# Performance work log

Hardware: AMD Instinct MI355X
Metric: run time of the kernel (lower is better)

The kernel has to match this reference:

```python
import jax, jax.numpy as jnp
import numpy as np

N = 16384
D = 512
K = 1024          # fixed num_clusters (torch code uses randint(2, N//2))
NUM_ITERS = 10    # kmeans Lloyd iterations
NUM_CLUSTER_ITERS = 1
TEMPERATURE = 0.1
CONCENTRATION = 0.1
EPS = 1e-6


def setup_inputs() -> dict:
    key = jax.random.key(0)
    feats = jax.random.normal(key, (N, D), dtype=jnp.float32)
    return {"feats": feats}


def _assign(feats, centroids, x_sq):
    c_sq = jnp.sum(centroids * centroids, axis=-1)            # [K]
    d = x_sq[:, None] - 2.0 * (feats @ centroids.T) + c_sq[None, :]
    return jnp.argmin(d, axis=-1)                             # [N] int32


def _kmeans(feats, num_clusters, num_iters):
    x_sq = jnp.sum(feats * feats, axis=-1)                    # [N]
    init_centroids = feats[:num_clusters]                     # deterministic init

    def body(_, centroids):
        clusters = _assign(feats, centroids, x_sq)
        sums = jax.ops.segment_sum(feats, clusters, num_segments=num_clusters)
        counts = jax.ops.segment_sum(jnp.ones((feats.shape[0],), feats.dtype),
                                     clusters, num_segments=num_clusters)
        new_c = sums / jnp.maximum(counts, 1.0)[:, None]
        # keep old centroid for empty clusters
        return jnp.where(counts[:, None] > 0, new_c, centroids)

    centroids = jax.lax.fori_loop(0, num_iters, body, init_centroids)
    clusters = _assign(feats, centroids, x_sq)
    counts = jax.ops.segment_sum(jnp.ones((feats.shape[0],), feats.dtype),
                                 clusters, num_segments=num_clusters)
    return clusters, centroids, counts


def reference(feats):
    clusters, centroids, _ = _kmeans(feats, K, NUM_ITERS)
    # per-point squared residuals gathered by cluster id, scatter-added to [K, D]
    resid2 = (feats - centroids[clusters]) ** 2               # [N, D]
    dists = jax.ops.segment_sum(resid2, clusters, num_segments=K)  # [K, D]
    # entropy loss branch (concentration phi)
    p = jnp.exp(-dists / CONCENTRATION)
    Q = p / jnp.sum(p)
    entropy = jnp.mean(Q * jnp.log(Q + EPS)) / NUM_CLUSTER_ITERS
    # nll branch (temperature t)
    p2 = jnp.exp(-dists / TEMPERATURE)
    nll = -jnp.mean(jnp.log(p2 + EPS))
    return entropy + nll
```

## Files before the change

kernel.cpp:

```cpp
#include <hip/hip_runtime.h>
#include <math.h>

#define N 16384
#define D 512
#define K 1024
#define NUM_ITERS 10
#define TEMPERATURE 0.1f
#define CONCENTRATION 0.1f
#define EPS 1e-6f

typedef unsigned short ushort_t;
typedef unsigned int uint_t;
typedef unsigned long long u64;
typedef __attribute__((ext_vector_type(4))) float floatx4;
typedef __attribute__((ext_vector_type(8))) short shortx8;

#define BM 128
#define BN 128
#define BK 64

__device__ inline ushort_t f2h(float f) {
    _Float16 h = (_Float16)f;
    return *(ushort_t*)&h;
}

__device__ inline unsigned ford(float f) {
    unsigned b = __float_as_uint(f);
    return (b & 0x80000000u) ? ~b : (b | 0x80000000u);
}

__device__ inline void f4add(float4& a, const float4& b) {
    a.x += b.x; a.y += b.y; a.z += b.z; a.w += b.w;
}

__device__ inline void gld16(const void* g, void* l) {
    __builtin_amdgcn_global_load_lds(
        (const __attribute__((address_space(1))) void*)(uintptr_t)(g),
        (__attribute__((address_space(3))) void*)(uintptr_t)(l), 16, 0, 0);
}

__global__ void split_kernel(const float* __restrict__ x, ushort_t* __restrict__ hi,
                             u64* __restrict__ best2, int n4) {
    int i = blockIdx.x * 256 + threadIdx.x;
    if (i >= n4) return;
    float4 v = ((const float4*)x)[i];
    ushort4 hv = {f2h(v.x), f2h(v.y), f2h(v.z), f2h(v.w)};
    ((ushort4*)hi)[i] = hv;
    if (i < 2 * N) best2[i] = ~0ull;
}

__global__ void rowsq_kernel(const float* __restrict__ x, float* __restrict__ out, int rows) {
    int row = blockIdx.x * 4 + (threadIdx.x >> 6);
    int lane = threadIdx.x & 63;
    if (row >= rows) return;
    const float* r = x + (size_t)row * D;
    float s = 0.f;
    for (int i = lane; i < D; i += 64) { float v = r[i]; s += v * v; }
    for (int off = 32; off > 0; off >>= 1) s += __shfl_down(s, off, 64);
    if (lane == 0) out[row] = s;
}

__global__ __launch_bounds__(256) void assign_mfma(
    const ushort_t* __restrict__ Ah, const ushort_t* __restrict__ Bh,
    const float* __restrict__ csq, u64* __restrict__ best)
{
    __shared__ __align__(16) ushort_t sAh[BM * BK];
    __shared__ __align__(16) ushort_t sBh[BN * BK];

    const int tid = threadIdx.x;
    const int lane = tid & 63;
    const int wave = tid >> 6;
    const int wr = wave >> 1, wc = wave & 1;
    const int quad = lane >> 4, l16 = lane & 15;

    const int q = (int)blockIdx.x;
    const int xid = q & 7;
    const int s = q >> 3;
    const int brow = ((s >> 3) << 3) + xid;
    const int bcol = s & 7;
    const int row0 = brow * BM, col0 = bcol * BN;

    floatx4 acc[4][4];
#pragma unroll
    for (int a = 0; a < 4; ++a)
#pragma unroll
        for (int b = 0; b < 4; ++b) acc[a][b] = (floatx4){0.f, 0.f, 0.f, 0.f};

    const int r_s0 = tid >> 3;
    const int kb_s0 = tid & 7;

    for (int d0 = 0; d0 < D; d0 += BK) {
        __syncthreads();
#pragma unroll
        for (int i = 0; i < 4; ++i) {
            const int row = r_s0 + i * 32;
            const int kb = kb_s0 ^ (row & 7);
            const int dst = (i * 256 + tid) * 8;
            const size_t ga = (size_t)(row0 + row) * D + d0 + kb * 8;
            const size_t gb = (size_t)(col0 + row) * D + d0 + kb * 8;
            gld16(Ah + ga, sAh + dst);
            gld16(Bh + gb, sBh + dst);
        }
        __syncthreads();

#pragma unroll
        for (int c = 0; c < 2; ++c) {
            shortx8 fah[4], fbh[4];
#pragma unroll
            for (int t = 0; t < 4; ++t) {
                const int ar = wr * 64 + t * 16 + l16;
                const int bc = wc * 64 + t * 16 + l16;
                const int kbl = c * 4 + quad;
                const int qa = (kbl ^ (ar & 7)) * 8;
                const int qb = (kbl ^ (bc & 7)) * 8;
                fah[t] = *(const shortx8*)&sAh[ar * BK + qa];
                fbh[t] = *(const shortx8*)&sBh[bc * BK + qb];
            }
#pragma unroll
            for (int i = 0; i < 4; ++i)
#pragma unroll
                for (int j = 0; j < 4; ++j)
                    acc[i][j] = __builtin_amdgcn_mfma_f32_16x16x32_f16(fah[i], fbh[j], acc[i][j], 0, 0, 0);
        }
    }

    float csqv[4];
#pragma unroll
    for (int j = 0; j < 4; ++j) csqv[j] = csq[col0 + wc * 64 + j * 16 + l16];

    const int k0 = col0 + wc * 64 + l16;
#pragma unroll
    for (int i = 0; i < 4; ++i) {
#pragma unroll
        for (int r = 0; r < 4; ++r) {
            float bv = csqv[0] - 2.0f * acc[i][0][r];
            int bk = k0;
#pragma unroll
            for (int j = 1; j < 4; ++j) {
                float v = csqv[j] - 2.0f * acc[i][j][r];
                int kk = k0 + j * 16;
                if (v < bv || (v == bv && kk < bk)) { bv = v; bk = kk; }
            }
#pragma unroll
            for (int m = 1; m < 16; m <<= 1) {
                float ov = __shfl_xor(bv, m, 64);
                int ok = __shfl_xor(bk, m, 64);
                if (ov < bv || (ov == bv && ok < bk)) { bv = ov; bk = ok; }
            }
            if (l16 == 0) {
                int p = row0 + wr * 64 + i * 16 + quad * 4 + r;
                u64 pk = ((u64)ford(bv) << 32) | (unsigned)bk;
                atomicMin(&best[p], pk);
            }
        }
    }
}

#define CU_WAVES 8
#define CHUNKS (N / 128)
#define ROUNDS 4
#define WIN (CHUNKS / ROUNDS)
#define CPW (WIN / CU_WAVES)

__global__ __launch_bounds__(512) void cluster_update(
    const float* __restrict__ feats, const u64* __restrict__ best,
    u64* __restrict__ best_other,
    float* __restrict__ cent, ushort_t* __restrict__ Bh,
    float* __restrict__ csq)
{
    __shared__ int list[CU_WAVES][CPW * 128];
    __shared__ int lcnt[CU_WAVES];
    __shared__ float4 part[CU_WAVES][64][2];
    __shared__ int pcnt_s[CU_WAVES];

    const int tid = threadIdx.x;
    const int lane = tid & 63;
    const int wave = tid >> 6;
    const int k = (int)blockIdx.x;

    float4 a0 = {0.f, 0.f, 0.f, 0.f}, a1 = {0.f, 0.f, 0.f, 0.f};
    int cnttot = 0;

    for (int round = 0; round < ROUNDS; ++round) {
        int cw = 0;
#pragma unroll
        for (int cc = 0; cc < CPW; ++cc) {
            int chunk = round * WIN + wave * CPW + cc;
            ulonglong2 v = ((const ulonglong2*)best)[chunk * 64 + lane];
            int id0 = (int)(uint_t)v.x;
            int id1 = (int)(uint_t)v.y;
            int p0 = chunk * 128 + 2 * lane;
            u64 m0 = __ballot(id0 == k);
            u64 m1 = __ballot(id1 == k);
            int c0 = __popcll(m0);
            u64 lanem = (1ull << lane) - 1ull;
            if (id0 == k) list[wave][cw + __popcll(m0 & lanem)] = p0;
            if (id1 == k) list[wave][cw + c0 + __popcll(m1 & lanem)] = p0 + 1;
            cw += c0 + __popcll(m1);
        }
        if (lane == 0) lcnt[wave] = cw;
        cnttot += cw;
        __syncthreads();

        int off[CU_WAVES]; int T = 0;
#pragma unroll
        for (int j = 0; j < CU_WAVES; ++j) { off[j] = T; T += lcnt[j]; }

        for (int g0 = wave; g0 < T; g0 += CU_WAVES * 4) {
            int nb = 0; int pidx[4];
#pragma unroll
            for (int b = 0; b < 4; ++b) {
                int g = g0 + CU_WAVES * b;
                if (g < T) {
                    int j = 0;
#pragma unroll
                    for (int jj = 1; jj < CU_WAVES; ++jj) if (g >= off[jj]) j = jj;
                    pidx[nb++] = list[j][g - off[j]];
                }
            }
            float4 x[4][2];
#pragma unroll
            for (int b = 0; b < 4; ++b) if (b < nb) {
                const float4* r = (const float4*)(feats + (size_t)pidx[b] * D) + lane * 2;
                x[b][0] = r[0]; x[b][1] = r[1];
            }
#pragma unroll
            for (int b = 0; b < 4; ++b) if (b < nb) {
                f4add(a0, x[b][0]); f4add(a1, x[b][1]);
            }
        }
        __syncthreads();
    }

    part[wave][lane][0] = a0; part[wave][lane][1] = a1;
    if (lane == 0) pcnt_s[wave] = cnttot;
    __syncthreads();

    if (wave == 0) {
        float4 s0 = part[0][lane][0], s1 = part[0][lane][1];
        int c = pcnt_s[0];
#pragma unroll
        for (int w = 1; w < CU_WAVES; ++w) {
            f4add(s0, part[w][lane][0]); f4add(s1, part[w][lane][1]);
            c += pcnt_s[w];
        }

        float4* crow = (float4*)(cent + (size_t)k * D) + lane * 2;
        float4 c0, c1;
        if (c > 0) {
            float cf = (float)c;
            c0 = (float4){s0.x / cf, s0.y / cf, s0.z / cf, s0.w / cf};
            c1 = (float4){s1.x / cf, s1.y / cf, s1.z / cf, s1.w / cf};
        } else {
            c0 = crow[0]; c1 = crow[1];
        }
        crow[0] = c0; crow[1] = c1;

        ushort4 hv;
        hv.x = f2h(c0.x); hv.y = f2h(c0.y); hv.z = f2h(c0.z); hv.w = f2h(c0.w);
        ((ushort4*)(Bh + (size_t)k * D))[lane * 2] = hv;
        hv.x = f2h(c1.x); hv.y = f2h(c1.y); hv.z = f2h(c1.z); hv.w = f2h(c1.w);
        ((ushort4*)(Bh + (size_t)k * D))[lane * 2 + 1] = hv;

        float s = c0.x * c0.x + c0.y * c0.y + c0.z * c0.z + c0.w * c0.w
                + c1.x * c1.x + c1.y * c1.y + c1.z * c1.z + c1.w * c1.w;
        for (int o = 32; o > 0; o >>= 1) s += __shfl_xor(s, o, 64);
        if (lane == 0) csq[k] = s;
    }

    if (tid < 16) best_other[k * 16 + tid] = ~0ull;
}

__global__ __launch_bounds__(512) void dist_gather(
    const float* __restrict__ feats, const float* __restrict__ cent,
    const u64* __restrict__ best, float* __restrict__ dists)
{
    __shared__ int list[CU_WAVES][CPW * 128];
    __shared__ int lcnt[CU_WAVES];
    __shared__ float4 part[CU_WAVES][64][2];

    const int tid = threadIdx.x;
    const int lane = tid & 63;
    const int wave = tid >> 6;
    const int k = (int)blockIdx.x;

    const float4* crow = (const float4*)(cent + (size_t)k * D) + lane * 2;
    const float4 c0 = crow[0], c1 = crow[1];

    float4 a0 = {0.f, 0.f, 0.f, 0.f}, a1 = {0.f, 0.f, 0.f, 0.f};

    for (int round = 0; round < ROUNDS; ++round) {
        int cw = 0;
#pragma unroll
        for (int cc = 0; cc < CPW; ++cc) {
            int chunk = round * WIN + wave * CPW + cc;
            ulonglong2 v = ((const ulonglong2*)best)[chunk * 64 + lane];
            int id0 = (int)(uint_t)v.x;
            int id1 = (int)(uint_t)v.y;
            int p0 = chunk * 128 + 2 * lane;
            u64 m0 = __ballot(id0 == k);
            u64 m1 = __ballot(id1 == k);
            int cc0 = __popcll(m0);
            u64 lanem = (1ull << lane) - 1ull;
            if (id0 == k) list[wave][cw + __popcll(m0 & lanem)] = p0;
            if (id1 == k) list[wave][cw + cc0 + __popcll(m1 & lanem)] = p0 + 1;
            cw += cc0 + __popcll(m1);
        }
        if (lane == 0) lcnt[wave] = cw;
        __syncthreads();

        int off[CU_WAVES]; int T = 0;
#pragma unroll
        for (int j = 0; j < CU_WAVES; ++j) { off[j] = T; T += lcnt[j]; }

        for (int g0 = wave; g0 < T; g0 += CU_WAVES * 4) {
            int nb = 0; int pidx[4];
#pragma unroll
            for (int b = 0; b < 4; ++b) {
                int g = g0 + CU_WAVES * b;
                if (g < T) {
                    int j = 0;
#pragma unroll
                    for (int jj = 1; jj < CU_WAVES; ++jj) if (g >= off[jj]) j = jj;
                    pidx[nb++] = list[j][g - off[j]];
                }
            }
            float4 x[4][2];
#pragma unroll
            for (int b = 0; b < 4; ++b) if (b < nb) {
                const float4* r = (const float4*)(feats + (size_t)pidx[b] * D) + lane * 2;
                x[b][0] = r[0]; x[b][1] = r[1];
            }
#pragma unroll
            for (int b = 0; b < 4; ++b) if (b < nb) {
                float r;
                r = x[b][0].x - c0.x; a0.x += r * r;  r = x[b][0].y - c0.y; a0.y += r * r;
                r = x[b][0].z - c0.z; a0.z += r * r;  r = x[b][0].w - c0.w; a0.w += r * r;
                r = x[b][1].x - c1.x; a1.x += r * r;  r = x[b][1].y - c1.y; a1.y += r * r;
                r = x[b][1].z - c1.z; a1.z += r * r;  r = x[b][1].w - c1.w; a1.w += r * r;
            }
        }
        __syncthreads();
    }

    part[wave][lane][0] = a0; part[wave][lane][1] = a1;
    __syncthreads();
    if (wave == 0) {
        float4 s0 = part[0][lane][0], s1 = part[0][lane][1];
#pragma unroll
        for (int w = 1; w < CU_WAVES; ++w) { f4add(s0, part[w][lane][0]); f4add(s1, part[w][lane][1]); }
        float4* drow = (float4*)(dists + (size_t)k * D) + lane * 2;
        drow[0] = s0; drow[1] = s1;
    }
}

__global__ void sump_kernel(const float* __restrict__ dists, double* __restrict__ S) {
    int tid = threadIdx.x;
    float v = 0.f;
    for (int idx = blockIdx.x * 256 + tid; idx < K * D; idx += 256 * 256)
        v += expf(-(dists[idx] / CONCENTRATION));
    __shared__ float red[4];
    for (int off = 32; off > 0; off >>= 1) v += __shfl_down(v, off, 64);
    if ((tid & 63) == 0) red[tid >> 6] = v;
    __syncthreads();
    if (tid == 0) atomicAdd(S, (double)(red[0] + red[1] + red[2] + red[3]));
}

__global__ void loss_kernel(const float* __restrict__ dists, const double* __restrict__ Sd,
                            double* __restrict__ acc2) {
    int tid = threadIdx.x;
    float S = (float)Sd[0];
    float e = 0.f, nl = 0.f;
    for (int idx = blockIdx.x * 256 + tid; idx < K * D; idx += 256 * 256) {
        float dv = dists[idx];
        float p = expf(-(dv / CONCENTRATION));
        float qq = p / S;
        e += qq * logf(qq + EPS);
        float p2 = expf(-(dv / TEMPERATURE));
        nl += logf(p2 + EPS);
    }
    __shared__ float rede[4];
    __shared__ float redn[4];
    for (int off = 32; off > 0; off >>= 1) { e += __shfl_down(e, off, 64); nl += __shfl_down(nl, off, 64); }
    if ((tid & 63) == 0) { rede[tid >> 6] = e; redn[tid >> 6] = nl; }
    __syncthreads();
    if (tid == 0) {
        atomicAdd(&acc2[0], (double)(rede[0] + rede[1] + rede[2] + rede[3]));
        atomicAdd(&acc2[1], (double)(redn[0] + redn[1] + redn[2] + redn[3]));
    }
}

__global__ void finalize_kernel(const double* __restrict__ acc2, float* __restrict__ out) {
    double kd = (double)(K * D);
    double entropy = acc2[0] / kd;
    double nll = -(acc2[1] / kd);
    out[0] = (float)(entropy + nll);
}

extern "C" void kernel_launch(void* const* d_in, const int* in_sizes, int n_in,
                              void* d_out, int out_size, void* d_ws, size_t ws_size,
                              hipStream_t stream) {
    const float* feats = (const float*)d_in[0];
    float* out = (float*)d_out;

    ushort_t* Ah = (ushort_t*)d_ws;
    ushort_t* Bh = Ah + (size_t)N * D;
    float* centroids = (float*)(Bh + (size_t)K * D);
    float* dists     = centroids + (size_t)K * D;
    float* csq       = dists + (size_t)K * D;
    u64*   best0     = (u64*)(csq + K);
    u64*   best1     = best0 + N;
    double* scal     = (double*)(best1 + N);

    split_kernel<<<(N * D / 4) / 256, 256, 0, stream>>>(feats, Ah, best0, N * D / 4);
    hipMemcpyAsync(centroids, feats, (size_t)K * D * sizeof(float),
                   hipMemcpyDeviceToDevice, stream);
    rowsq_kernel<<<K / 4, 256, 0, stream>>>(feats, csq, K);

    for (int it = 0; it < NUM_ITERS; ++it) {
        u64* cur = (it & 1) ? best1 : best0;
        u64* oth = (it & 1) ? best0 : best1;
        const ushort_t* bh = (it == 0) ? Ah : Bh;
        assign_mfma<<<(N / BM) * (K / BN), 256, 0, stream>>>(Ah, bh, csq, cur);
        cluster_update<<<K, 512, 0, stream>>>(feats, cur, oth, centroids, Bh, csq);
    }
    u64* fin = (NUM_ITERS & 1) ? best1 : best0;
    assign_mfma<<<(N / BM) * (K / BN), 256, 0, stream>>>(Ah, Bh, csq, fin);

    dist_gather<<<K, 512, 0, stream>>>(feats, centroids, fin, dists);

    hipMemsetAsync(scal, 0, 3 * sizeof(double), stream);
    sump_kernel<<<256, 256, 0, stream>>>(dists, &scal[0]);
    loss_kernel<<<256, 256, 0, stream>>>(dists, &scal[0], &scal[1]);
    finalize_kernel<<<1, 1, 0, stream>>>(&scal[1], out);
}
```

Baseline: 773.5 us.

## Rewrite assign GEMM with 256x256 tiles and multi-stage async LDS pipeline

Replaces the 128x128, 256-thread assignment GEMM with a 256x256-tile, 512-thread kernel. The new kernel prefetches K-slices into four LDS buffers several stages ahead using global_load_lds, with explicit vmcnt waits and barriers. It also uses a new swizzle and raises MFMA priority around the compute bursts. The aim is to hide global-load latency, raise data reuse per tile, and cut the barrier stalls of the old load-then-compute loop. The cost is a larger LDS footprint (64 KB) and more accumulator registers, which may limit occupancy. The hand-counted waitcnt values also carry correctness risk.

```diff
diff --git a/kernel.cpp b/kernel.cpp
--- a/kernel.cpp
+++ b/kernel.cpp
@@ -15,10 +15,6 @@
 typedef __attribute__((ext_vector_type(4))) float floatx4;
 typedef __attribute__((ext_vector_type(8))) short shortx8;
 
-#define BM 128
-#define BN 128
-#define BK 64
-
 __device__ inline ushort_t f2h(float f) {
     _Float16 h = (_Float16)f;
     return *(ushort_t*)&h;
@@ -38,6 +34,8 @@
         (const __attribute__((address_space(1))) void*)(uintptr_t)(g),
         (__attribute__((address_space(3))) void*)(uintptr_t)(l), 16, 0, 0);
 }
+
+#define WAITVM(n_lit) asm volatile("s_waitcnt vmcnt(" #n_lit ")" ::: "memory")
 
 __global__ void split_kernel(const float* __restrict__ x, ushort_t* __restrict__ hi,
                              u64* __restrict__ best2, int n4) {
@@ -60,67 +58,95 @@
     if (lane == 0) out[row] = s;
 }
 
-__global__ __launch_bounds__(256) void assign_mfma(
+__global__ __launch_bounds__(512, 2) void assign_mfma2(
     const ushort_t* __restrict__ Ah, const ushort_t* __restrict__ Bh,
     const float* __restrict__ csq, u64* __restrict__ best)
 {
-    __shared__ __align__(16) ushort_t sAh[BM * BK];
-    __shared__ __align__(16) ushort_t sBh[BN * BK];
+    __shared__ __align__(16) ushort_t sA[4][8192];
+    __shared__ __align__(16) ushort_t sB[4][8192];
 
     const int tid = threadIdx.x;
     const int lane = tid & 63;
     const int wave = tid >> 6;
-    const int wr = wave >> 1, wc = wave & 1;
+    const int wr = wave >> 2, wc = wave & 3;
     const int quad = lane >> 4, l16 = lane & 15;
 
-    const int q = (int)blockIdx.x;
-    const int xid = q & 7;
-    const int s = q >> 3;
-    const int brow = ((s >> 3) << 3) + xid;
-    const int bcol = s & 7;
-    const int row0 = brow * BM, col0 = bcol * BN;
-
-    floatx4 acc[4][4];
-#pragma unroll
-    for (int a = 0; a < 4; ++a)
+    const int bid = (int)blockIdx.x;
+    const int xid = bid & 7;
+    const int s = bid >> 3;
+    const int brow = (xid << 3) + (s >> 2);
+    const int bcol = s & 3;
+    const int row0 = brow * 256, col0 = bcol * 256;
+
+    floatx4 acc[8][4];
+#pragma unroll
+    for (int a = 0; a < 8; ++a)
 #pragma unroll
         for (int b = 0; b < 4; ++b) acc[a][b] = (floatx4){0.f, 0.f, 0.f, 0.f};
 
-    const int r_s0 = tid >> 3;
-    const int kb_s0 = tid & 7;
-
-    for (int d0 = 0; d0 < D; d0 += BK) {
-        __syncthreads();
-#pragma unroll
-        for (int i = 0; i < 4; ++i) {
-            const int row = r_s0 + i * 32;
-            const int kb = kb_s0 ^ (row & 7);
-            const int dst = (i * 256 + tid) * 8;
-            const size_t ga = (size_t)(row0 + row) * D + d0 + kb * 8;
-            const size_t gb = (size_t)(col0 + row) * D + d0 + kb * 8;
-            gld16(Ah + ga, sAh + dst);
-            gld16(Bh + gb, sBh + dst);
-        }
-        __syncthreads();
-
-#pragma unroll
-        for (int c = 0; c < 2; ++c) {
-            shortx8 fah[4], fbh[4];
-#pragma unroll
-            for (int t = 0; t < 4; ++t) {
-                const int ar = wr * 64 + t * 16 + l16;
-                const int bc = wc * 64 + t * 16 + l16;
-                const int kbl = c * 4 + quad;
-                const int qa = (kbl ^ (ar & 7)) * 8;
-                const int qb = (kbl ^ (bc & 7)) * 8;
-                fah[t] = *(const shortx8*)&sAh[ar * BK + qa];
-                fbh[t] = *(const shortx8*)&sBh[bc * BK + qb];
-            }
+    const int swz = (quad ^ (l16 & 3) ^ ((l16 >> 2) & 3)) * 8;
+    const int aoff = (wr * 128 + l16) * 32 + swz;
+    const int boff = (wc * 64 + l16) * 32 + swz;
+
+    auto stage = [&](int h) {
+        const int u_h = h >> 2;
+        const int part = h & 3;
+        const int kh = part >> 1;
+        const int reg = ((u_h & 1) << 1) | kh;
+        const int d_off = u_h * 64 + kh * 32;
+        const ushort_t* src = (part & 1) ? Bh : Ah;
+        const int r0 = (part & 1) ? col0 : row0;
+        ushort_t* dstreg = (part & 1) ? &sB[reg][0] : &sA[reg][0];
+#pragma unroll
+        for (int ii = 0; ii < 2; ++ii) {
+            const int idx = ii * 512 + tid;
+            const int row = idx >> 2;
+            const int kb = (idx & 3) ^ (row & 3) ^ ((row >> 2) & 3);
+            gld16(src + (size_t)(r0 + row) * D + d_off + kb * 8, dstreg + idx * 8);
+        }
+    };
+
+    #pragma unroll
+    for (int h = 0; h < 6; ++h) stage(h);
+    WAITVM(8);
+    __builtin_amdgcn_s_barrier();
+    __builtin_amdgcn_sched_barrier(0);
+
+    shortx8 fb[4];
+#pragma unroll
+    for (int u = 0; u < 8; ++u) {
+        const int rbase = (u & 1) << 1;
+#pragma unroll
+        for (int p = 0; p < 4; ++p) {
+            const int g = u * 4 + p;
+            if (g + 6 < 32) stage(g + 6);
+            const int kh = p >> 1;
+            const int ih = p & 1;
+            const ushort_t* Areg = &sA[rbase + kh][0];
+            const ushort_t* Breg = &sB[rbase + kh][0];
+            shortx8 fa[4];
+            if (ih == 0) {
+#pragma unroll
+                for (int j = 0; j < 4; ++j) fb[j] = *(const shortx8*)&Breg[boff + j * 512];
+            }
+#pragma unroll
+            for (int i = 0; i < 4; ++i) fa[i] = *(const shortx8*)&Areg[aoff + (ih * 4 + i) * 512];
+            __builtin_amdgcn_s_setprio(1);
 #pragma unroll
             for (int i = 0; i < 4; ++i)
 #pragma unroll
                 for (int j = 0; j < 4; ++j)
-                    acc[i][j] = __builtin_amdgcn_mfma_f32_16x16x32_f16(fah[i], fbh[j], acc[i][j], 0, 0, 0);
+                    acc[ih * 4 + i][j] = __builtin_amdgcn_mfma_f32_16x16x32_f16(
+                        fa[i], fb[j], acc[ih * 4 + i][j], 0, 0, 0);
+            __builtin_amdgcn_s_setprio(0);
+            if ((p == 1 || p == 3) && !(u == 7 && p == 3)) {
+                asm volatile("s_waitcnt lgkmcnt(0)" ::: "memory");
+                if (u == 7 && p == 1)      { WAITVM(0); }
+                else if (u == 6 && p == 3) { WAITVM(4); }
+                else                       { WAITVM(8); }
+                __builtin_amdgcn_s_barrier();
+                __builtin_amdgcn_sched_barrier(0);
+            }
         }
     }
 
@@ -130,7 +156,7 @@
 
     const int k0 = col0 + wc * 64 + l16;
 #pragma unroll
-    for (int i = 0; i < 4; ++i) {
+    for (int i = 0; i < 8; ++i) {
 #pragma unroll
         for (int r = 0; r < 4; ++r) {
             float bv = csqv[0] - 2.0f * acc[i][0][r];
@@ -148,7 +174,7 @@
                 if (ov < bv || (ov == bv && ok < bk)) { bv = ov; bk = ok; }
             }
             if (l16 == 0) {
-                int p = row0 + wr * 64 + i * 16 + quad * 4 + r;
+                int p = row0 + wr * 128 + i * 16 + quad * 4 + r;
                 u64 pk = ((u64)ford(bv) << 32) | (unsigned)bk;
                 atomicMin(&best[p], pk);
             }
@@ -421,11 +447,11 @@
         u64* cur = (it & 1) ? best1 : best0;
         u64* oth = (it & 1) ? best0 : best1;
         const ushort_t* bh = (it == 0) ? Ah : Bh;
-        assign_mfma<<<(N / BM) * (K / BN), 256, 0, stream>>>(Ah, bh, csq, cur);
+        assign_mfma2<<<(N / 256) * (K / 256), 512, 0, stream>>>(Ah, bh, csq, cur);
         cluster_update<<<K, 512, 0, stream>>>(feats, cur, oth, centroids, Bh, csq);
     }
     u64* fin = (NUM_ITERS & 1) ? best1 : best0;
-    assign_mfma<<<(N / BM) * (K / BN), 256, 0, stream>>>(Ah, Bh, csq, fin);
+    assign_mfma2<<<(N / 256) * (K / 256), 512, 0, stream>>>(Ah, Bh, csq, fin);
 
     dist_gather<<<K, 512, 0, stream>>>(feats, centroids, fin, dists);
 
```

Result: faster. 703.0 us (-9.1%).
